# Performance work log

Measured on AMD Instinct MI355X. Metric: run time of the kernel, lower is better.

## Reference

```python
import jax, jax.numpy as jnp
import numpy as np

D_MODEL = 768
NUM_HEADS = 12
D_K = D_MODEL // NUM_HEADS


def setup_inputs() -> dict:
    key = jax.random.key(0)
    ks = jax.random.split(key, 11)
    B, L = 1, 4096
    s = 1.0 / np.sqrt(D_MODEL)
    return {
        "q": jax.random.normal(ks[0], (B, L, D_MODEL), jnp.float32),
        "k": jax.random.normal(ks[1], (B, L, D_MODEL), jnp.float32),
        "v": jax.random.normal(ks[2], (B, L, D_MODEL), jnp.float32),
        "Wq": jax.random.normal(ks[3], (D_MODEL, D_MODEL), jnp.float32) * s,
        "bq": jax.random.normal(ks[4], (D_MODEL,), jnp.float32) * s,
        "Wk": jax.random.normal(ks[5], (D_MODEL, D_MODEL), jnp.float32) * s,
        "bk": jax.random.normal(ks[6], (D_MODEL,), jnp.float32) * s,
        "Wv": jax.random.normal(ks[7], (D_MODEL, D_MODEL), jnp.float32) * s,
        "bv": jax.random.normal(ks[8], (D_MODEL,), jnp.float32) * s,
        "Wo": jax.random.normal(ks[9], (D_MODEL, D_MODEL), jnp.float32) * s,
        "bo": jax.random.normal(ks[10], (D_MODEL,), jnp.float32) * s,
    }


def reference(q, k, v, Wq, bq, Wk, bk, Wv, bv, Wo, bo):
    B, L, _ = q.shape
    # linear projections (torch Linear: x @ W.T + b)
    qp = q @ Wq.T + bq
    kp = k @ Wk.T + bk
    vp = v @ Wv.T + bv
    # split heads: (B, H, L, d_k)
    def split(x):
        return x.reshape(B, L, NUM_HEADS, D_K).transpose(0, 2, 1, 3)
    qh, kh, vh = split(qp), split(kp), split(vp)
    scale = 1.0 / jnp.sqrt(jnp.asarray(D_K, qh.dtype))
    scores = jnp.einsum("bhqd,bhkd->bhqk", qh, kh) * scale  # (B,H,L,L)
    weights = jax.nn.softmax(scores, axis=-1)
    out = jnp.einsum("bhqk,bhkd->bhqd", weights, vh)
    out = out.transpose(0, 2, 1, 3).reshape(B, L, D_MODEL)
    return out @ Wo.T + bo
```

## Files before the change

### kernel.cpp

```cpp
#include <hip/hip_runtime.h>
#include <stdint.h>
#include <math.h>

#define L_SEQ  4096
#define DMODEL 768
#define NHEADS 12
#define DKH    64
#define QSCALE 0.18033688011112042f

typedef _Float16 f16;
typedef __attribute__((ext_vector_type(8))) _Float16 half8;
typedef __attribute__((ext_vector_type(4))) _Float16 half4;
typedef __attribute__((ext_vector_type(4))) float f32x4;
typedef __attribute__((ext_vector_type(16))) float f32x16;
typedef __attribute__((ext_vector_type(4))) unsigned int uint4v;

#define MFMA16(a, b, c) __builtin_amdgcn_mfma_f32_16x16x32_f16(a, b, c, 0, 0, 0)
#define MFMA32(a, b, c) __builtin_amdgcn_mfma_f32_32x32x16_f16(a, b, c, 0, 0, 0)

#define NE ((size_t)L_SEQ * DMODEL)
#define WE ((size_t)DMODEL * DMODEL)

static __device__ __forceinline__ unsigned int pack2(float a, float b) {
  return __builtin_bit_cast(unsigned int, __builtin_amdgcn_cvt_pkrtz(a, b));
}

__global__ __launch_bounds__(256)
void cvt_all(const float* __restrict__ q, const float* __restrict__ k,
             const float* __restrict__ v, const float* __restrict__ Wq,
             const float* __restrict__ Wk, const float* __restrict__ Wv,
             const float* __restrict__ Wo, f16* __restrict__ x16,
             f16* __restrict__ w16)
{
  const size_t NE4 = NE / 4, WE4 = WE / 4;
  size_t i = (size_t)blockIdx.x * 256 + threadIdx.x;
  const float* srcs[7] = {q, k, v, Wq, Wk, Wv, Wo};
  f16* dsts[7] = {x16, x16 + NE, x16 + 2 * NE,
                  w16, w16 + WE, w16 + 2 * WE, w16 + 3 * WE};
  const size_t sz4[7] = {NE4, NE4, NE4, WE4, WE4, WE4, WE4};
  int r = 0; size_t off = i;
  while (off >= sz4[r]) { off -= sz4[r]; ++r; }
  float4 f = reinterpret_cast<const float4*>(srcs[r])[off];
  half4 h; h[0] = (f16)f.x; h[1] = (f16)f.y; h[2] = (f16)f.z; h[3] = (f16)f.w;
  reinterpret_cast<half4*>(dsts[r])[off] = h;
}

__global__ __launch_bounds__(256)
void qkv_gemm(const f16* __restrict__ x16, const f16* __restrict__ w16,
              const float* __restrict__ bq, const float* __restrict__ bk,
              const float* __restrict__ bv,
              f16* __restrict__ Qp, f16* __restrict__ Kp, f16* __restrict__ VpT)
{
  __shared__ f16 As[128][72];
  __shared__ f16 Bs[128][72];
  const int tid  = threadIdx.x;
  const int lane = tid & 63, wid = tid >> 6;
  const int lq   = lane & 15, quad = lane >> 4;
  const int wm   = (wid & 1) * 64, wn = (wid >> 1) * 64;

  const int d   = blockIdx.x;
  const int r8  = d & 7;
  const int j   = d >> 3;
  const int g   = r8 + 8 * (j / 6);
  const int nb  = j % 6;
  const int widx = g / 32;
  const int m0   = (g % 32) * 128;
  const int n0   = nb * 128;

  const f16* X = x16 + (size_t)widx * NE;
  const f16* W = w16 + (size_t)widx * WE;
  const float* Bv = (widx == 0) ? bq : (widx == 1) ? bk : bv;

  const int srow = tid >> 1, sseg = (tid & 1) * 32;
  const f16* aptr = X + (size_t)(m0 + srow) * DMODEL + sseg;
  const f16* bptr = W + (size_t)(n0 + srow) * DMODEL + sseg;

  half8 a4[4], b4[4];
#pragma unroll
  for (int u = 0; u < 4; ++u) {
    a4[u] = reinterpret_cast<const half8*>(aptr)[u];
    b4[u] = reinterpret_cast<const half8*>(bptr)[u];
  }

  f32x4 acc[4][4] = {};

  for (int k0 = 0; k0 < DMODEL; k0 += 64) {
#pragma unroll
    for (int u = 0; u < 4; ++u) {
      *reinterpret_cast<half8*>(&As[srow][sseg + u * 8]) = a4[u];
      *reinterpret_cast<half8*>(&Bs[srow][sseg + u * 8]) = b4[u];
    }
    __syncthreads();

    if (k0 + 64 < DMODEL) {
#pragma unroll
      for (int u = 0; u < 4; ++u) {
        a4[u] = reinterpret_cast<const half8*>(aptr + k0 + 64)[u];
        b4[u] = reinterpret_cast<const half8*>(bptr + k0 + 64)[u];
      }
    }

#pragma unroll
    for (int ks = 0; ks < 2; ++ks) {
      half8 bf[4];
#pragma unroll
      for (int nf = 0; nf < 4; ++nf)
        bf[nf] = *reinterpret_cast<half8*>(&Bs[wn + nf * 16 + lq][ks * 32 + quad * 8]);
#pragma unroll
      for (int mf = 0; mf < 4; ++mf) {
        half8 af = *reinterpret_cast<half8*>(&As[wm + mf * 16 + lq][ks * 32 + quad * 8]);
#pragma unroll
        for (int nf = 0; nf < 4; ++nf)
          acc[mf][nf] = MFMA16(af, bf[nf], acc[mf][nf]);
      }
    }
    __syncthreads();
  }

#pragma unroll
  for (int nf = 0; nf < 4; ++nf) {
    const int col  = n0 + wn + nf * 16 + lq;
    const float bias = Bv[col];
#pragma unroll
    for (int mf = 0; mf < 4; ++mf) {
      const int rowb = m0 + wm + mf * 16 + quad * 4;
      if (widx == 2) {
        half4 o4;
#pragma unroll
        for (int r = 0; r < 4; ++r) o4[r] = (f16)(acc[mf][nf][r] + bias);
        *reinterpret_cast<half4*>(VpT + (size_t)col * L_SEQ + rowb) = o4;
      } else if (widx == 0) {
#pragma unroll
        for (int r = 0; r < 4; ++r)
          Qp[(size_t)(rowb + r) * DMODEL + col] = (f16)((acc[mf][nf][r] + bias) * QSCALE);
      } else {
#pragma unroll
        for (int r = 0; r < 4; ++r)
          Kp[(size_t)(rowb + r) * DMODEL + col] = (f16)(acc[mf][nf][r] + bias);
      }
    }
  }
}

__global__ __launch_bounds__(256, 3)
void attn_mfma4(const f16* __restrict__ Qp, const f16* __restrict__ Kp,
                const f16* __restrict__ VpT, f16* __restrict__ AO)
{
  const int h  = blockIdx.x;
  const int q0 = blockIdx.y * 64;
  const int tid  = threadIdx.x;
  const int lane = tid & 63, wid = tid >> 6;
  const int l31  = lane & 31, hc = lane >> 5;
  const int qh   = wid & 1, kh = wid >> 1;

  __shared__ __align__(16) char smem[36864];
  f16 (*Ks)[64][72] = (f16 (*)[64][72])smem;
  f16 (*Vt)[64][72] = (f16 (*)[64][72])(smem + 18432);
  float* Of  = (float*)smem;
  float* lf  = (float*)(smem + 16384);
  f16*   Of16 = (f16*)(smem + 16640);

  half8 qf[4];
#pragma unroll
  for (int st = 0; st < 4; ++st)
    qf[st] = *reinterpret_cast<const half8*>(
        Qp + (size_t)(q0 + qh * 32 + l31) * DMODEL + h * DKH + st * 16 + hc * 8);

  f32x16 oacc[2] = {};
  float lsum = 0.0f;

  const int srow = tid >> 2, sseg = (tid & 3) * 16;
  const f16* kbase = Kp  + (size_t)srow * DMODEL + h * DKH + sseg;
  const f16* vbase = VpT + (size_t)(h * DKH + srow) * L_SEQ + sseg;

  half8 k0 = *reinterpret_cast<const half8*>(kbase);
  half8 k1 = *reinterpret_cast<const half8*>(kbase + 8);
  half8 v0 = *reinterpret_cast<const half8*>(vbase);
  half8 v1 = *reinterpret_cast<const half8*>(vbase + 8);

  int p = 0;
  for (int kt = 0; kt < L_SEQ; kt += 64) {
    *reinterpret_cast<half8*>(&Ks[p][srow][sseg])     = k0;
    *reinterpret_cast<half8*>(&Ks[p][srow][sseg + 8]) = k1;
    *reinterpret_cast<half8*>(&Vt[p][srow][sseg])     = v0;
    *reinterpret_cast<half8*>(&Vt[p][srow][sseg + 8]) = v1;
    __syncthreads();

    if (kt + 64 < L_SEQ) {
      const f16* kn = kbase + (size_t)(kt + 64) * DMODEL;
      const f16* vn = vbase + (kt + 64);
      k0 = *reinterpret_cast<const half8*>(kn);
      k1 = *reinterpret_cast<const half8*>(kn + 8);
      v0 = *reinterpret_cast<const half8*>(vn);
      v1 = *reinterpret_cast<const half8*>(vn + 8);
    }

    __builtin_amdgcn_s_setprio(1);

    f32x16 s = {};
#pragma unroll
    for (int st = 0; st < 4; ++st) {
      half8 kf = *reinterpret_cast<half8*>(&Ks[p][kh * 32 + l31][st * 16 + hc * 8]);
      s = MFMA32(kf, qf[st], s);
    }

    unsigned int pk[8];
#pragma unroll
    for (int i = 0; i < 8; ++i) {
      float p0 = __builtin_amdgcn_exp2f(s[2 * i]);
      float p1 = __builtin_amdgcn_exp2f(s[2 * i + 1]);
      lsum += p0 + p1;
      pk[i] = pack2(p0, p1);
    }

#pragma unroll
    for (int st = 0; st < 2; ++st) {
      unsigned int w0 = pk[4 * st + 0], w1 = pk[4 * st + 1];
      unsigned int w2 = pk[4 * st + 2], w3 = pk[4 * st + 3];
      asm("v_permlane32_swap_b32 %0, %1" : "+v"(w0), "+v"(w2));
      asm("v_permlane32_swap_b32 %0, %1" : "+v"(w1), "+v"(w3));
      uint4v pw; pw[0] = w0; pw[1] = w1; pw[2] = w2; pw[3] = w3;
      half8 pf = __builtin_bit_cast(half8, pw);
#pragma unroll
      for (int a = 0; a < 2; ++a) {
        half8 vf = *reinterpret_cast<half8*>(&Vt[p][a * 32 + l31][kh * 32 + st * 16 + hc * 8]);
        oacc[a] = MFMA32(vf, pf, oacc[a]);
      }
    }
    __builtin_amdgcn_s_setprio(0);
    p ^= 1;
  }
  __syncthreads();

  float lw = lsum + __shfl_xor(lsum, 32);

  if (kh == 0) {
#pragma unroll
    for (int a = 0; a < 2; ++a)
#pragma unroll
      for (int r = 0; r < 16; ++r) {
        int d = a * 32 + (r & 3) + 8 * (r >> 2) + 4 * hc;
        Of[((qh * 64) + d) * 32 + l31] = oacc[a][r];
      }
    if (lane < 32) lf[qh * 32 + l31] = lw;
  }
  __syncthreads();
  if (kh == 1) {
    const float inv = 1.0f / (lf[qh * 32 + l31] + lw);
#pragma unroll
    for (int a = 0; a < 2; ++a)
#pragma unroll
      for (int r = 0; r < 16; ++r) {
        int d = a * 32 + (r & 3) + 8 * (r >> 2) + 4 * hc;
        float val = (Of[((qh * 64) + d) * 32 + l31] + oacc[a][r]) * inv;
        Of16[(qh * 32 + l31) * 64 + d] = (f16)val;
      }
  }
  __syncthreads();

  *reinterpret_cast<half8*>(AO + (size_t)(q0 + srow) * DMODEL + h * DKH + sseg) =
      *reinterpret_cast<half8*>(&Of16[srow * 64 + sseg]);
  *reinterpret_cast<half8*>(AO + (size_t)(q0 + srow) * DMODEL + h * DKH + sseg + 8) =
      *reinterpret_cast<half8*>(&Of16[srow * 64 + sseg + 8]);
}

__global__ __launch_bounds__(256)
void out_gemm(const f16* __restrict__ A, const f16* __restrict__ W,
              const float* __restrict__ Bv, float* __restrict__ O)
{
  __shared__ f16 As[128][72];
  __shared__ f16 Bs[128][72];
  const int tid  = threadIdx.x;
  const int lane = tid & 63, wid = tid >> 6;
  const int lq   = lane & 15, quad = lane >> 4;
  const int wm   = (wid & 1) * 64, wn = (wid >> 1) * 64;

  const int d   = blockIdx.x;
  const int r8  = d & 7;
  const int j   = d >> 3;
  const int g   = r8 + 8 * (j / 6);
  const int nb  = j % 6;
  const int m0  = g * 128, n0 = nb * 128;

  const int srow = tid >> 1, sseg = (tid & 1) * 32;
  const f16* aptr = A + (size_t)(m0 + srow) * DMODEL + sseg;
  const f16* bptr = W + (size_t)(n0 + srow) * DMODEL + sseg;

  half8 a4[4], b4[4];
#pragma unroll
  for (int u = 0; u < 4; ++u) {
    a4[u] = reinterpret_cast<const half8*>(aptr)[u];
    b4[u] = reinterpret_cast<const half8*>(bptr)[u];
  }

  f32x4 acc[4][4] = {};

  for (int k0 = 0; k0 < DMODEL; k0 += 64) {
#pragma unroll
    for (int u = 0; u < 4; ++u) {
      *reinterpret_cast<half8*>(&As[srow][sseg + u * 8]) = a4[u];
      *reinterpret_cast<half8*>(&Bs[srow][sseg + u * 8]) = b4[u];
    }
    __syncthreads();

    if (k0 + 64 < DMODEL) {
#pragma unroll
      for (int u = 0; u < 4; ++u) {
        a4[u] = reinterpret_cast<const half8*>(aptr + k0 + 64)[u];
        b4[u] = reinterpret_cast<const half8*>(bptr + k0 + 64)[u];
      }
    }

#pragma unroll
    for (int ks = 0; ks < 2; ++ks) {
      half8 bf[4];
#pragma unroll
      for (int nf = 0; nf < 4; ++nf)
        bf[nf] = *reinterpret_cast<half8*>(&Bs[wn + nf * 16 + lq][ks * 32 + quad * 8]);
#pragma unroll
      for (int mf = 0; mf < 4; ++mf) {
        half8 af = *reinterpret_cast<half8*>(&As[wm + mf * 16 + lq][ks * 32 + quad * 8]);
#pragma unroll
        for (int nf = 0; nf < 4; ++nf)
          acc[mf][nf] = MFMA16(af, bf[nf], acc[mf][nf]);
      }
    }
    __syncthreads();
  }

#pragma unroll
  for (int nf = 0; nf < 4; ++nf) {
    const int col = n0 + wn + nf * 16 + lq;
    const float bias = Bv[col];
#pragma unroll
    for (int mf = 0; mf < 4; ++mf) {
      const int rowb = m0 + wm + mf * 16 + quad * 4;
#pragma unroll
      for (int r = 0; r < 4; ++r)
        O[(size_t)(rowb + r) * DMODEL + col] = acc[mf][nf][r] + bias;
    }
  }
}

extern "C" void kernel_launch(void* const* d_in, const int* in_sizes, int n_in,
                              void* d_out, int out_size, void* d_ws, size_t ws_size,
                              hipStream_t stream) {
  const float* q  = (const float*)d_in[0];
  const float* k  = (const float*)d_in[1];
  const float* v  = (const float*)d_in[2];
  const float* Wq = (const float*)d_in[3];
  const float* bq = (const float*)d_in[4];
  const float* Wk = (const float*)d_in[5];
  const float* bk = (const float*)d_in[6];
  const float* Wv = (const float*)d_in[7];
  const float* bv = (const float*)d_in[8];
  const float* Wo = (const float*)d_in[9];
  const float* bo = (const float*)d_in[10];
  float* out = (float*)d_out;

  f16* x16 = (f16*)d_ws;
  f16* w16 = x16 + 3 * NE;
  f16* Qp  = w16 + 4 * WE;
  f16* Kp  = Qp + NE;
  f16* VpT = Kp + NE;
  f16* AO  = VpT + NE;

  const int ncvt = (int)((3 * (NE / 4) + 4 * (WE / 4)) / 256);
  cvt_all<<<ncvt, 256, 0, stream>>>(q, k, v, Wq, Wk, Wv, Wo, x16, w16);

  qkv_gemm<<<576, 256, 0, stream>>>(x16, w16, bq, bk, bv, Qp, Kp, VpT);

  dim3 gattn(NHEADS, L_SEQ / 64);
  attn_mfma4<<<gattn, 256, 0, stream>>>(Qp, Kp, VpT, AO);

  out_gemm<<<192, 256, 0, stream>>>(AO, w16 + 3 * WE, bo, out);
}
```

Baseline: 224.5 us.

## Load K/V MFMA fragments directly from global into registers, dropping LDS staging

The attention kernel no longer stages K and V tiles through shared memory with a per-tile barrier. Each wave now loads its own MFMA operand fragments straight from global memory into registers, double-buffered across two key tiles, and the main loop is unrolled by two. This removes the LDS writes and reads and the __syncthreads in the inner loop, and shrinks shared memory. In exchange, the waves sharing a key half each fetch the same K/V data separately, so global and L2 traffic rise, the V loads become narrower strided accesses, and register pressure grows.

Result: slower. 323.6 us (+44.1%).

```diff
diff --git a/kernel.cpp b/kernel.cpp
--- a/kernel.cpp
+++ b/kernel.cpp
@@ -142,6 +142,46 @@
   }
 }
 
+#define LOADK(dst, kt)                                                        \
+  { _Pragma("unroll") for (int st = 0; st < 4; ++st)                          \
+      dst[st] = *reinterpret_cast<const half8*>(                              \
+          kptr + (size_t)(kt) * DMODEL + st * 16); }
+
+#define LOADV(dst, kt)                                                        \
+  { _Pragma("unroll") for (int a = 0; a < 2; ++a)                             \
+    _Pragma("unroll") for (int st = 0; st < 2; ++st)                          \
+      dst[2 * a + st] = *reinterpret_cast<const half8*>(                      \
+          vptr + (size_t)a * 32 * L_SEQ + (kt) + st * 16); }
+
+#define ATTN_STEP(kk, vv)                                                     \
+  {                                                                           \
+    __builtin_amdgcn_s_setprio(1);                                            \
+    f32x16 s = {};                                                            \
+    _Pragma("unroll")                                                         \
+    for (int st = 0; st < 4; ++st) s = MFMA32(kk[st], qf[st], s);             \
+    unsigned int pk[8];                                                       \
+    _Pragma("unroll")                                                         \
+    for (int i = 0; i < 8; ++i) {                                             \
+      float p0 = __builtin_amdgcn_exp2f(s[2 * i]);                            \
+      float p1 = __builtin_amdgcn_exp2f(s[2 * i + 1]);                        \
+      lsum += p0 + p1;                                                        \
+      pk[i] = pack2(p0, p1);                                                  \
+    }                                                                         \
+    _Pragma("unroll")                                                         \
+    for (int st = 0; st < 2; ++st) {                                          \
+      unsigned int w0 = pk[4 * st + 0], w1 = pk[4 * st + 1];                  \
+      unsigned int w2 = pk[4 * st + 2], w3 = pk[4 * st + 3];                  \
+      asm("v_permlane32_swap_b32 %0, %1" : "+v"(w0), "+v"(w2));               \
+      asm("v_permlane32_swap_b32 %0, %1" : "+v"(w1), "+v"(w3));               \
+      uint4v pw; pw[0] = w0; pw[1] = w1; pw[2] = w2; pw[3] = w3;              \
+      half8 pf = __builtin_bit_cast(half8, pw);                               \
+      _Pragma("unroll")                                                       \
+      for (int a = 0; a < 2; ++a)                                             \
+        oacc[a] = MFMA32(vv[2 * a + st], pf, oacc[a]);                        \
+    }                                                                         \
+    __builtin_amdgcn_s_setprio(0);                                            \
+  }
+
 __global__ __launch_bounds__(256, 3)
 void attn_mfma4(const f16* __restrict__ Qp, const f16* __restrict__ Kp,
                 const f16* __restrict__ VpT, f16* __restrict__ AO)
@@ -153,9 +193,7 @@
   const int l31  = lane & 31, hc = lane >> 5;
   const int qh   = wid & 1, kh = wid >> 1;
 
-  __shared__ __align__(16) char smem[36864];
-  f16 (*Ks)[64][72] = (f16 (*)[64][72])smem;
-  f16 (*Vt)[64][72] = (f16 (*)[64][72])(smem + 18432);
+  __shared__ __align__(16) char smem[25088];
   float* Of  = (float*)smem;
   float* lf  = (float*)(smem + 16384);
   f16*   Of16 = (f16*)(smem + 16640);
@@ -169,68 +207,20 @@
   f32x16 oacc[2] = {};
   float lsum = 0.0f;
 
-  const int srow = tid >> 2, sseg = (tid & 3) * 16;
-  const f16* kbase = Kp  + (size_t)srow * DMODEL + h * DKH + sseg;
-  const f16* vbase = VpT + (size_t)(h * DKH + srow) * L_SEQ + sseg;
-
-  half8 k0 = *reinterpret_cast<const half8*>(kbase);
-  half8 k1 = *reinterpret_cast<const half8*>(kbase + 8);
-  half8 v0 = *reinterpret_cast<const half8*>(vbase);
-  half8 v1 = *reinterpret_cast<const half8*>(vbase + 8);
-
-  int p = 0;
-  for (int kt = 0; kt < L_SEQ; kt += 64) {
-    *reinterpret_cast<half8*>(&Ks[p][srow][sseg])     = k0;
-    *reinterpret_cast<half8*>(&Ks[p][srow][sseg + 8]) = k1;
-    *reinterpret_cast<half8*>(&Vt[p][srow][sseg])     = v0;
-    *reinterpret_cast<half8*>(&Vt[p][srow][sseg + 8]) = v1;
-    __syncthreads();
-
-    if (kt + 64 < L_SEQ) {
-      const f16* kn = kbase + (size_t)(kt + 64) * DMODEL;
-      const f16* vn = vbase + (kt + 64);
-      k0 = *reinterpret_cast<const half8*>(kn);
-      k1 = *reinterpret_cast<const half8*>(kn + 8);
-      v0 = *reinterpret_cast<const half8*>(vn);
-      v1 = *reinterpret_cast<const half8*>(vn + 8);
-    }
-
-    __builtin_amdgcn_s_setprio(1);
-
-    f32x16 s = {};
-#pragma unroll
-    for (int st = 0; st < 4; ++st) {
-      half8 kf = *reinterpret_cast<half8*>(&Ks[p][kh * 32 + l31][st * 16 + hc * 8]);
-      s = MFMA32(kf, qf[st], s);
-    }
-
-    unsigned int pk[8];
-#pragma unroll
-    for (int i = 0; i < 8; ++i) {
-      float p0 = __builtin_amdgcn_exp2f(s[2 * i]);
-      float p1 = __builtin_amdgcn_exp2f(s[2 * i + 1]);
-      lsum += p0 + p1;
-      pk[i] = pack2(p0, p1);
-    }
-
-#pragma unroll
-    for (int st = 0; st < 2; ++st) {
-      unsigned int w0 = pk[4 * st + 0], w1 = pk[4 * st + 1];
-      unsigned int w2 = pk[4 * st + 2], w3 = pk[4 * st + 3];
-      asm("v_permlane32_swap_b32 %0, %1" : "+v"(w0), "+v"(w2));
-      asm("v_permlane32_swap_b32 %0, %1" : "+v"(w1), "+v"(w3));
-      uint4v pw; pw[0] = w0; pw[1] = w1; pw[2] = w2; pw[3] = w3;
-      half8 pf = __builtin_bit_cast(half8, pw);
-#pragma unroll
-      for (int a = 0; a < 2; ++a) {
-        half8 vf = *reinterpret_cast<half8*>(&Vt[p][a * 32 + l31][kh * 32 + st * 16 + hc * 8]);
-        oacc[a] = MFMA32(vf, pf, oacc[a]);
-      }
-    }
-    __builtin_amdgcn_s_setprio(0);
-    p ^= 1;
-  }
-  __syncthreads();
+  const f16* kptr = Kp  + (size_t)(kh * 32 + l31) * DMODEL + h * DKH + hc * 8;
+  const f16* vptr = VpT + (size_t)(h * DKH + l31) * L_SEQ + kh * 32 + hc * 8;
+
+  half8 ka[4], va[4], kb[4], vb[4];
+  LOADK(ka, 0); LOADV(va, 0);
+
+  for (int kt = 0; kt < L_SEQ; kt += 128) {
+    LOADK(kb, kt + 64); LOADV(vb, kt + 64);
+    ATTN_STEP(ka, va);
+    if (kt + 128 < L_SEQ) {
+      LOADK(ka, kt + 128); LOADV(va, kt + 128);
+    }
+    ATTN_STEP(kb, vb);
+  }
 
   float lw = lsum + __shfl_xor(lsum, 32);
 
@@ -258,6 +248,7 @@
   }
   __syncthreads();
 
+  const int srow = tid >> 2, sseg = (tid & 3) * 16;
   *reinterpret_cast<half8*>(AO + (size_t)(q0 + srow) * DMODEL + h * DKH + sseg) =
       *reinterpret_cast<half8*>(&Of16[srow * 64 + sseg]);
   *reinterpret_cast<half8*>(AO + (size_t)(q0 + srow) * DMODEL + h * DKH + sseg + 8) =
```
